# Kernel optimization log

Hardware: AMD Instinct MI355X
Metric: run time of the kernel (lower is better)

Reference implementation:

```python
import jax, jax.numpy as jnp
import numpy as np
import math

DENOM = 32.0

# e3nn scalar_activation normalizes the activation to unit second moment under N(0,1).
# Compute the gelu normalization constant by Gauss-Hermite quadrature.
_zs, _ws = np.polynomial.hermite_e.hermegauss(64)
_g = 0.5 * _zs * (1.0 + np.array([math.erf(z / math.sqrt(2.0)) for z in _zs]))
C_GELU = float(1.0 / math.sqrt((_ws * _g * _g).sum() / math.sqrt(2.0 * math.pi)))


def _spherical_harmonics(r):
    # r: [E,3] unit vectors. Component-normalized real SH for l=1,2,3.
    x, y, z = r[..., 0], r[..., 1], r[..., 2]
    s3, s5, s15 = math.sqrt(3.0), math.sqrt(5.0), math.sqrt(15.0)
    s7, s105 = math.sqrt(7.0), math.sqrt(105.0)
    s35_8, s21_8 = math.sqrt(35.0 / 8.0), math.sqrt(21.0 / 8.0)
    Y1 = s3 * r                                                     # [E,3]
    Y2 = jnp.stack([s15 * x * y, s15 * y * z, 0.5 * s5 * (3 * z * z - 1),
                    s15 * x * z, 0.5 * s15 * (x * x - y * y)], -1)   # [E,5]
    Y3 = jnp.stack([s35_8 * y * (3 * x * x - y * y), s105 * x * y * z,
                    s21_8 * y * (5 * z * z - 1), 0.5 * s7 * z * (5 * z * z - 3),
                    s21_8 * x * (5 * z * z - 1), 0.5 * s105 * z * (x * x - y * y),
                    s35_8 * x * (x * x - 3 * y * y)], -1)            # [E,7]
    return [Y1, Y2, Y3]


def setup_inputs() -> dict:
    key = jax.random.key(0)
    k = jax.random.split(key, 7)
    N, E, MUL, TMUL = 32768, 1048576, 16, 32
    return {
        "x": jax.random.normal(k[0], (N, MUL), jnp.float32),
        "positions": jax.random.normal(k[1], (N, 3), jnp.float32),
        "W_pre": jax.random.normal(k[2], (4, MUL, TMUL), jnp.float32),
        "W_post": jax.random.normal(k[3], (4, TMUL, TMUL), jnp.float32),
        "W_shortcut": jax.random.normal(k[4], (MUL, TMUL), jnp.float32),
        "senders": jax.random.randint(k[5], (E,), 0, N, jnp.int32),
        "receivers": jax.random.randint(k[6], (E,), 0, N, jnp.int32),
    }


def reference(x, positions, W_pre, W_post, W_shortcut, senders, receivers):
    N, mul = x.shape
    tmul = W_pre.shape[-1]
    # --- edge update: sh of relative positions, tensor product with sender scalars ---
    rvec = positions[receivers] - positions[senders]                 # [E,3]
    n = jnp.linalg.norm(rvec, axis=-1, keepdims=True)
    rhat = rvec / jnp.where(n == 0, 1.0, n)
    Ys = _spherical_harmonics(rhat)
    s = x[senders]                                                   # [E,mul] (0e)
    # --- aggregate edge features at receivers (segment sum) ---
    agg = [jax.ops.segment_sum(s, receivers, num_segments=N)]        # 0e block
    for Y in Ys:
        e = (s[:, :, None] * Y[:, None, :]).reshape(s.shape[0], -1)  # 0e x l -> l
        agg.append(jax.ops.segment_sum(e, receivers, num_segments=N).reshape(N, mul, Y.shape[-1]))
    # --- node update: linear_pre -> scalar act -> linear_post, plus shortcut ---
    inv_in = 1.0 / math.sqrt(mul)
    inv_mid = 1.0 / math.sqrt(tmul)
    out = []
    for l in range(4):
        a = agg[l] / DENOM
        if l == 0:
            p = (a @ W_pre[0]) * inv_in
            p = C_GELU * jax.nn.gelu(p, approximate=False)           # act on 0e scalars only
            q = (p @ W_post[0]) * inv_mid
            q = q + (x @ W_shortcut) * inv_in                        # shortcut: only 0e path exists
            out.append(q)
        else:
            p = jnp.einsum('nui,uv->nvi', a, W_pre[l]) * inv_in
            q = jnp.einsum('nvi,vw->nwi', p, W_post[l]) * inv_mid
            out.append(q.reshape(N, -1))
    return jnp.concatenate(out, axis=-1)                              # [N, tmul*16]
```

## Files before the change

kernel.cpp:

```cpp
#include <hip/hip_runtime.h>
#include <math.h>

#define NN 32768
#define EN 1048576
#define NBIN 256
#define BINCAP 8192
#define TILE 4096

#define C_GELU_F 1.5335262f

__global__ __launch_bounds__(256) void bin_k(const int* __restrict__ snd,
                                             const int* __restrict__ rcv,
                                             int* __restrict__ bin_cur,
                                             unsigned* __restrict__ binbuf) {
    __shared__ unsigned cnt[NBIN];
    __shared__ unsigned excl[NBIN];
    __shared__ unsigned cur2[NBIN];
    __shared__ unsigned gbase[NBIN];
    __shared__ unsigned stage[TILE];
    int t = threadIdx.x;
    int tile = blockIdx.x * TILE;
    cnt[t] = 0; cur2[t] = 0;
    __syncthreads();

    unsigned w[TILE / 256];
#pragma unroll
    for (int i = 0; i < TILE / 256; ++i) {
        int e = tile + i * 256 + t;
        unsigned r = (unsigned)rcv[e], s = (unsigned)snd[e];
        w[i] = (r << 15) | s;
        atomicAdd(&cnt[w[i] >> 22], 1u);
    }
    __syncthreads();

    unsigned my = cnt[t];
    excl[t] = my;
    __syncthreads();
    for (int d = 1; d < NBIN; d <<= 1) {
        unsigned v = (t >= d) ? excl[t - d] : 0u;
        __syncthreads();
        excl[t] += v;
        __syncthreads();
    }
    unsigned myexcl = excl[t] - my;
    gbase[t] = atomicAdd((unsigned*)&bin_cur[t], my);
    __syncthreads();
    excl[t] = myexcl;
    __syncthreads();

#pragma unroll
    for (int i = 0; i < TILE / 256; ++i) {
        unsigned b = w[i] >> 22;
        unsigned p = excl[b] + atomicAdd(&cur2[b], 1u);
        stage[p] = w[i];
    }
    __syncthreads();

    for (int p = t; p < TILE; p += 256) {
        unsigned ww = stage[p];
        unsigned b = ww >> 22;
        unsigned idx = gbase[b] + ((unsigned)p - excl[b]);
        if (idx < BINCAP) binbuf[b * BINCAP + idx] = ww;
    }
}

__global__ __launch_bounds__(256) void scan_k(const int* __restrict__ bin_cur,
                                              int* __restrict__ bin_start) {
    __shared__ unsigned sc[NBIN];
    int t = threadIdx.x;
    unsigned my = (unsigned)bin_cur[t];
    sc[t] = my;
    __syncthreads();
    for (int d = 1; d < NBIN; d <<= 1) {
        unsigned v = (t >= d) ? sc[t - d] : 0u;
        __syncthreads();
        sc[t] += v;
        __syncthreads();
    }
    bin_start[t] = (int)(sc[t] - my);
}

__global__ __launch_bounds__(256) void csr_k(const int* __restrict__ bin_cur,
                                             const int* __restrict__ bin_start,
                                             const unsigned* __restrict__ binbuf,
                                             int* __restrict__ row_ptr,
                                             int* __restrict__ edge_csr) {
    __shared__ unsigned cnt[128];
    __shared__ unsigned excl[128];
    __shared__ unsigned cur2[128];
    int b = blockIdx.x;
    int t = threadIdx.x;
    int M = bin_cur[b]; M = M > BINCAP ? BINCAP : M;
    int base = bin_start[b];
    if (t < 128) { cnt[t] = 0; cur2[t] = 0; }
    __syncthreads();

    const unsigned* bb = binbuf + b * BINCAP;
    for (int i = t; i < M; i += 256)
        atomicAdd(&cnt[(bb[i] >> 15) & 127], 1u);
    __syncthreads();

    if (t < 128) excl[t] = cnt[t];
    __syncthreads();
    for (int d = 1; d < 128; d <<= 1) {
        unsigned v = (t >= d && t < 128) ? excl[t - d] : 0u;
        __syncthreads();
        if (t < 128) excl[t] += v;
        __syncthreads();
    }
    if (t < 128) {
        unsigned e = excl[t] - cnt[t];
        excl[t] = e;
        row_ptr[(b << 7) + t] = base + (int)e;
        if (b == NBIN - 1 && t == 127) row_ptr[NN] = base + (int)(e + cnt[127]);
    }
    __syncthreads();

    for (int i = t; i < M; i += 256) {
        unsigned ww = bb[i];
        unsigned r7 = (ww >> 15) & 127;
        unsigned dst = excl[r7] + atomicAdd(&cur2[r7], 1u);
        edge_csr[base + dst] = (int)(ww & 0x7FFF);
    }
}

__global__ __launch_bounds__(256) void pos_k(const float* __restrict__ pos,
                                             float4* __restrict__ posw) {
    int n = blockIdx.x * 256 + threadIdx.x;
    posw[n] = make_float4(pos[3*n], pos[3*n+1], pos[3*n+2], 0.f);
}

#define TSTRIDE 17
#define NSTRIDE (16 * TSTRIDE)

__global__ __launch_bounds__(256) void fused_k(const float* __restrict__ x,
                                               const float4* __restrict__ posw,
                                               const int* __restrict__ row_ptr,
                                               const int* __restrict__ edge_csr,
                                               const float* __restrict__ Wpre,
                                               const float* __restrict__ Wpost,
                                               const float* __restrict__ Wsc,
                                               float* __restrict__ out) {
    __shared__ float sPre[4*516];
    __shared__ float sPost[4*1028];
    __shared__ float sSc[512];
    __shared__ float sT[16 * NSTRIDE];

    int t = threadIdx.x;
    for (int idx = t; idx < 2048; idx += 256)
        sPre[(idx >> 9)*516 + (idx & 511)] = Wpre[idx];
    for (int idx = t; idx < 4096; idx += 256)
        sPost[(idx >> 10)*1028 + (idx & 1023)] = Wpost[idx];
    sSc[t] = Wsc[t];
    sSc[t + 256] = Wsc[t + 256];

    int nl = t >> 4;
    int n  = blockIdx.x * 16 + nl;
    int u  = t & 15;
    int beg = row_ptr[n], end = row_ptr[n + 1];
    int cnt = end - beg;
    float4 rp = posw[n];
    float acc[16];
#pragma unroll
    for (int j = 0; j < 16; ++j) acc[j] = 0.f;

    const float s3   = 1.7320508075688772f;
    const float s5   = 2.2360679774997896f;
    const float s15  = 3.8729833462074170f;
    const float s7   = 2.6457513110645907f;
    const float s105 = 10.246950765959598f;
    const float s35_8 = 2.0916500663351889f;
    const float s21_8 = 1.6201851746019651f;

    int cl = cnt > 0 ? cnt - 1 : 0;
    int sA = edge_csr[beg];
    int sB = edge_csr[beg + (1 < cl ? 1 : cl)];
    float4 spA = posw[sA];
    float  xvA = x[(sA << 4) + u];

    for (int k = 0; k < cnt; ++k) {
        int    s  = sA;
        float4 sp = spA;
        float  sv = xvA;
        sA = sB;
        int k2 = k + 2; k2 = k2 < cl ? k2 : cl;
        sB = edge_csr[beg + k2];
        spA = posw[sA];
        xvA = x[(sA << 4) + u];

        float vx = rp.x - sp.x, vy = rp.y - sp.y, vz = rp.z - sp.z;
        float n2 = vx*vx + vy*vy + vz*vz;
        float inv;
        if (n2 > 0.f) {
            inv = rsqrtf(n2);
            inv = inv * (1.5f - 0.5f * n2 * inv * inv);
        } else inv = 0.f;
        float X = vx*inv, Y = vy*inv, Z = vz*inv;
        float XX = X*X, YY = Y*Y, ZZ = Z*Z;

        acc[0]  += sv;
        acc[1]  += sv * (s3*X);
        acc[2]  += sv * (s3*Y);
        acc[3]  += sv * (s3*Z);
        acc[4]  += sv * (s15*X*Y);
        acc[5]  += sv * (s15*Y*Z);
        acc[6]  += sv * (0.5f*s5*(3.f*ZZ - 1.f));
        acc[7]  += sv * (s15*X*Z);
        acc[8]  += sv * (0.5f*s15*(XX - YY));
        acc[9]  += sv * (s35_8*Y*(3.f*XX - YY));
        acc[10] += sv * (s105*X*Y*Z);
        acc[11] += sv * (s21_8*Y*(5.f*ZZ - 1.f));
        acc[12] += sv * (0.5f*s7*Z*(5.f*ZZ - 3.f));
        acc[13] += sv * (s21_8*X*(5.f*ZZ - 1.f));
        acc[14] += sv * (0.5f*s105*Z*(XX - YY));
        acc[15] += sv * (s35_8*X*(XX - 3.f*YY));
    }

    float* tp = sT + nl * NSTRIDE + u * TSTRIDE;
#pragma unroll
    for (int j = 0; j < 16; ++j) tp[j] = acc[j];
    __syncthreads();

    int j = t & 15;
    int l, i, offl, deg;
    if (j == 0)      { l = 0; i = 0;     offl = 0;   deg = 1; }
    else if (j < 4)  { l = 1; i = j - 1; offl = 32;  deg = 3; }
    else if (j < 9)  { l = 2; i = j - 4; offl = 128; deg = 5; }
    else             { l = 3; i = j - 9; offl = 288; deg = 7; }

    const float c1 = 0.0078125f;
    const float c2 = 0.17677669529663687f;

    const float* ap = sT + nl * NSTRIDE + j;
    float p[32];
#pragma unroll
    for (int v = 0; v < 32; ++v) p[v] = 0.f;
    const float* wp = sPre + l * 516;
#pragma unroll
    for (int uu = 0; uu < 16; ++uu) {
        float a = ap[uu * TSTRIDE];
        const float4* w4 = (const float4*)(wp + (uu << 5));
#pragma unroll
        for (int vq = 0; vq < 8; ++vq) {
            float4 w = w4[vq];
            p[4*vq+0] += a * w.x;
            p[4*vq+1] += a * w.y;
            p[4*vq+2] += a * w.z;
            p[4*vq+3] += a * w.w;
        }
    }
#pragma unroll
    for (int v = 0; v < 32; ++v) p[v] *= c1;

    if (j == 0) {
#pragma unroll
        for (int v = 0; v < 32; ++v) {
            float pv = p[v];
            p[v] = C_GELU_F * 0.5f * pv * (1.f + erff(pv * 0.7071067811865476f));
        }
    }

    float q[32];
#pragma unroll
    for (int w = 0; w < 32; ++w) q[w] = 0.f;
    const float* wq = sPost + l * 1028;
#pragma unroll
    for (int v = 0; v < 32; ++v) {
        float pv = p[v];
        const float4* w4 = (const float4*)(wq + (v << 5));
#pragma unroll
        for (int wd = 0; wd < 8; ++wd) {
            float4 w = w4[wd];
            q[4*wd+0] += pv * w.x;
            q[4*wd+1] += pv * w.y;
            q[4*wd+2] += pv * w.z;
            q[4*wd+3] += pv * w.w;
        }
    }
#pragma unroll
    for (int w = 0; w < 32; ++w) q[w] *= c2;

    if (j == 0) {
        const float* xp = x + (n << 4);
#pragma unroll
        for (int uu = 0; uu < 16; ++uu) {
            float xv = 0.25f * xp[uu];
            const float4* w4 = (const float4*)(sSc + (uu << 5));
#pragma unroll
            for (int wd = 0; wd < 8; ++wd) {
                float4 w = w4[wd];
                q[4*wd+0] += xv * w.x;
                q[4*wd+1] += xv * w.y;
                q[4*wd+2] += xv * w.z;
                q[4*wd+3] += xv * w.w;
            }
        }
    }

    float* op = out + (n << 9) + offl + i;
#pragma unroll
    for (int w = 0; w < 32; ++w) op[w * deg] = q[w];
}

extern "C" void kernel_launch(void* const* d_in, const int* in_sizes, int n_in,
                              void* d_out, int out_size, void* d_ws, size_t ws_size,
                              hipStream_t stream) {
    const float* x     = (const float*)d_in[0];
    const float* pos   = (const float*)d_in[1];
    const float* Wpre  = (const float*)d_in[2];
    const float* Wpost = (const float*)d_in[3];
    const float* Wsc   = (const float*)d_in[4];
    const int*   snd   = (const int*)d_in[5];
    const int*   rcv   = (const int*)d_in[6];
    float* out = (float*)d_out;

    char* ws = (char*)d_ws;
    int*      bin_cur   = (int*)(ws);
    int*      bin_start = (int*)(ws + 1024);
    int*      row_ptr   = (int*)(ws + 2048);
    float4*   posw      = (float4*)(ws + 0x30000);
    int*      edge_csr  = (int*)(ws + 0xB0000);
    unsigned* binbuf    = (unsigned*)(ws + 0x500000);

    hipMemsetAsync(bin_cur, 0, NBIN * sizeof(int), stream);
    bin_k<<<EN / TILE, 256, 0, stream>>>(snd, rcv, bin_cur, binbuf);
    scan_k<<<1, 256, 0, stream>>>(bin_cur, bin_start);
    csr_k<<<NBIN, 256, 0, stream>>>(bin_cur, bin_start, binbuf, row_ptr, edge_csr);
    pos_k<<<NN / 256, 256, 0, stream>>>(pos, posw);
    fused_k<<<NN / 16, 256, 0, stream>>>(x, posw, row_ptr, edge_csr,
                                         Wpre, Wpost, Wsc, out);
}
```

Baseline: 232.5 us.

## Parallelize edge SH across lanes and accumulate per-output-channel in fused kernel

The fused kernel now has each 16-lane group compute spherical harmonics for 16 edges in parallel, one edge per lane, and stage them in shared memory. Each lane then accumulates one SH component across all 16 input channels, with the sender id broadcast by shuffle and x read as float4 rows. This removes the redundant per-lane SH recomputation and the accumulator transpose through shared memory. Block sizes grow for the fused, binning and CSR kernels, at the cost of more registers and partial-chunk lane waste for low-degree nodes.

```diff
diff --git a/kernel.cpp b/kernel.cpp
--- a/kernel.cpp
+++ b/kernel.cpp
@@ -9,7 +9,7 @@
 
 #define C_GELU_F 1.5335262f
 
-__global__ __launch_bounds__(256) void bin_k(const int* __restrict__ snd,
+__global__ __launch_bounds__(512) void bin_k(const int* __restrict__ snd,
                                              const int* __restrict__ rcv,
                                              int* __restrict__ bin_cur,
                                              unsigned* __restrict__ binbuf) {
@@ -20,43 +20,44 @@
     __shared__ unsigned stage[TILE];
     int t = threadIdx.x;
     int tile = blockIdx.x * TILE;
-    cnt[t] = 0; cur2[t] = 0;
-    __syncthreads();
-
-    unsigned w[TILE / 256];
-#pragma unroll
-    for (int i = 0; i < TILE / 256; ++i) {
-        int e = tile + i * 256 + t;
+    if (t < NBIN) { cnt[t] = 0; cur2[t] = 0; }
+    __syncthreads();
+
+    unsigned w[TILE / 512];
+#pragma unroll
+    for (int i = 0; i < TILE / 512; ++i) {
+        int e = tile + i * 512 + t;
         unsigned r = (unsigned)rcv[e], s = (unsigned)snd[e];
         w[i] = (r << 15) | s;
         atomicAdd(&cnt[w[i] >> 22], 1u);
     }
     __syncthreads();
 
-    unsigned my = cnt[t];
-    excl[t] = my;
+    unsigned my = (t < NBIN) ? cnt[t] : 0u;
+    if (t < NBIN) excl[t] = my;
     __syncthreads();
     for (int d = 1; d < NBIN; d <<= 1) {
-        unsigned v = (t >= d) ? excl[t - d] : 0u;
-        __syncthreads();
-        excl[t] += v;
-        __syncthreads();
-    }
-    unsigned myexcl = excl[t] - my;
-    gbase[t] = atomicAdd((unsigned*)&bin_cur[t], my);
-    __syncthreads();
-    excl[t] = myexcl;
-    __syncthreads();
-
-#pragma unroll
-    for (int i = 0; i < TILE / 256; ++i) {
+        unsigned v = (t < NBIN && t >= d) ? excl[t - d] : 0u;
+        __syncthreads();
+        if (t < NBIN) excl[t] += v;
+        __syncthreads();
+    }
+    if (t < NBIN) {
+        unsigned myexcl = excl[t] - my;
+        gbase[t] = atomicAdd((unsigned*)&bin_cur[t], my);
+        excl[t] = myexcl;
+    }
+    __syncthreads();
+
+#pragma unroll
+    for (int i = 0; i < TILE / 512; ++i) {
         unsigned b = w[i] >> 22;
         unsigned p = excl[b] + atomicAdd(&cur2[b], 1u);
         stage[p] = w[i];
     }
     __syncthreads();
 
-    for (int p = t; p < TILE; p += 256) {
+    for (int p = t; p < TILE; p += 512) {
         unsigned ww = stage[p];
         unsigned b = ww >> 22;
         unsigned idx = gbase[b] + ((unsigned)p - excl[b]);
@@ -80,11 +81,11 @@
     bin_start[t] = (int)(sc[t] - my);
 }
 
-__global__ __launch_bounds__(256) void csr_k(const int* __restrict__ bin_cur,
-                                             const int* __restrict__ bin_start,
-                                             const unsigned* __restrict__ binbuf,
-                                             int* __restrict__ row_ptr,
-                                             int* __restrict__ edge_csr) {
+__global__ __launch_bounds__(1024) void csr_k(const int* __restrict__ bin_cur,
+                                              const int* __restrict__ bin_start,
+                                              const unsigned* __restrict__ binbuf,
+                                              int* __restrict__ row_ptr,
+                                              int* __restrict__ edge_csr) {
     __shared__ unsigned cnt[128];
     __shared__ unsigned excl[128];
     __shared__ unsigned cur2[128];
@@ -96,7 +97,7 @@
     __syncthreads();
 
     const unsigned* bb = binbuf + b * BINCAP;
-    for (int i = t; i < M; i += 256)
+    for (int i = t; i < M; i += 1024)
         atomicAdd(&cnt[(bb[i] >> 15) & 127], 1u);
     __syncthreads();
 
@@ -116,7 +117,7 @@
     }
     __syncthreads();
 
-    for (int i = t; i < M; i += 256) {
+    for (int i = t; i < M; i += 1024) {
         unsigned ww = bb[i];
         unsigned r7 = (ww >> 15) & 127;
         unsigned dst = excl[r7] + atomicAdd(&cur2[r7], 1u);
@@ -130,39 +131,38 @@
     posw[n] = make_float4(pos[3*n], pos[3*n+1], pos[3*n+2], 0.f);
 }
 
-#define TSTRIDE 17
-#define NSTRIDE (16 * TSTRIDE)
-
-__global__ __launch_bounds__(256) void fused_k(const float* __restrict__ x,
-                                               const float4* __restrict__ posw,
-                                               const int* __restrict__ row_ptr,
-                                               const int* __restrict__ edge_csr,
-                                               const float* __restrict__ Wpre,
-                                               const float* __restrict__ Wpost,
-                                               const float* __restrict__ Wsc,
-                                               float* __restrict__ out) {
+#define GROUPS 32
+#define BLK 512
+#define YST 20
+#define GST (16*YST + 8)
+
+__global__ __launch_bounds__(512, 4) void fused_k(const float* __restrict__ x,
+                                                  const float4* __restrict__ posw,
+                                                  const int* __restrict__ row_ptr,
+                                                  const int* __restrict__ edge_csr,
+                                                  const float* __restrict__ Wpre,
+                                                  const float* __restrict__ Wpost,
+                                                  const float* __restrict__ Wsc,
+                                                  float* __restrict__ out) {
     __shared__ float sPre[4*516];
     __shared__ float sPost[4*1028];
     __shared__ float sSc[512];
-    __shared__ float sT[16 * NSTRIDE];
+    __shared__ float sY[GROUPS * GST];
 
     int t = threadIdx.x;
-    for (int idx = t; idx < 2048; idx += 256)
+    for (int idx = t; idx < 2048; idx += BLK)
         sPre[(idx >> 9)*516 + (idx & 511)] = Wpre[idx];
-    for (int idx = t; idx < 4096; idx += 256)
+    for (int idx = t; idx < 4096; idx += BLK)
         sPost[(idx >> 10)*1028 + (idx & 1023)] = Wpost[idx];
     sSc[t] = Wsc[t];
-    sSc[t + 256] = Wsc[t + 256];
-
-    int nl = t >> 4;
-    int n  = blockIdx.x * 16 + nl;
-    int u  = t & 15;
+
+    int g = t >> 4;
+    int j = t & 15;
+    int n = blockIdx.x * GROUPS + g;
     int beg = row_ptr[n], end = row_ptr[n + 1];
     int cnt = end - beg;
     float4 rp = posw[n];
-    float acc[16];
-#pragma unroll
-    for (int j = 0; j < 16; ++j) acc[j] = 0.f;
+    float* yg = sY + g * GST;
 
     const float s3   = 1.7320508075688772f;
     const float s5   = 2.2360679774997896f;
@@ -172,22 +172,18 @@
     const float s35_8 = 2.0916500663351889f;
     const float s21_8 = 1.6201851746019651f;
 
-    int cl = cnt > 0 ? cnt - 1 : 0;
-    int sA = edge_csr[beg];
-    int sB = edge_csr[beg + (1 < cl ? 1 : cl)];
-    float4 spA = posw[sA];
-    float  xvA = x[(sA << 4) + u];
-
-    for (int k = 0; k < cnt; ++k) {
-        int    s  = sA;
-        float4 sp = spA;
-        float  sv = xvA;
-        sA = sB;
-        int k2 = k + 2; k2 = k2 < cl ? k2 : cl;
-        sB = edge_csr[beg + k2];
-        spA = posw[sA];
-        xvA = x[(sA << 4) + u];
-
+    float acc[16];
+#pragma unroll
+    for (int u = 0; u < 16; ++u) acc[u] = 0.f;
+
+    int nch = (cnt + 15) >> 4;
+    for (int c = 0; c < nch; ++c) {
+        int rem = cnt - (c << 4); rem = rem > 16 ? 16 : rem;
+
+        int k = (c << 4) + j;
+        int ki = k < cnt ? k : cnt - 1;
+        int sE = edge_csr[beg + ki];
+        float4 sp = posw[sE];
         float vx = rp.x - sp.x, vy = rp.y - sp.y, vz = rp.z - sp.z;
         float n2 = vx*vx + vy*vy + vz*vz;
         float inv;
@@ -198,30 +194,37 @@
         float X = vx*inv, Y = vy*inv, Z = vz*inv;
         float XX = X*X, YY = Y*Y, ZZ = Z*Z;
 
-        acc[0]  += sv;
-        acc[1]  += sv * (s3*X);
-        acc[2]  += sv * (s3*Y);
-        acc[3]  += sv * (s3*Z);
-        acc[4]  += sv * (s15*X*Y);
-        acc[5]  += sv * (s15*Y*Z);
-        acc[6]  += sv * (0.5f*s5*(3.f*ZZ - 1.f));
-        acc[7]  += sv * (s15*X*Z);
-        acc[8]  += sv * (0.5f*s15*(XX - YY));
-        acc[9]  += sv * (s35_8*Y*(3.f*XX - YY));
-        acc[10] += sv * (s105*X*Y*Z);
-        acc[11] += sv * (s21_8*Y*(5.f*ZZ - 1.f));
-        acc[12] += sv * (0.5f*s7*Z*(5.f*ZZ - 3.f));
-        acc[13] += sv * (s21_8*X*(5.f*ZZ - 1.f));
-        acc[14] += sv * (0.5f*s105*Z*(XX - YY));
-        acc[15] += sv * (s35_8*X*(XX - 3.f*YY));
-    }
-
-    float* tp = sT + nl * NSTRIDE + u * TSTRIDE;
-#pragma unroll
-    for (int j = 0; j < 16; ++j) tp[j] = acc[j];
-    __syncthreads();
-
-    int j = t & 15;
+        float* yr = yg + j * YST;
+        ((float4*)yr)[0] = make_float4(1.f, s3*X, s3*Y, s3*Z);
+        ((float4*)yr)[1] = make_float4(s15*X*Y, s15*Y*Z,
+                                       0.5f*s5*(3.f*ZZ - 1.f), s15*X*Z);
+        ((float4*)yr)[2] = make_float4(0.5f*s15*(XX - YY),
+                                       s35_8*Y*(3.f*XX - YY),
+                                       s105*X*Y*Z,
+                                       s21_8*Y*(5.f*ZZ - 1.f));
+        ((float4*)yr)[3] = make_float4(0.5f*s7*Z*(5.f*ZZ - 3.f),
+                                       s21_8*X*(5.f*ZZ - 1.f),
+                                       0.5f*s105*Z*(XX - YY),
+                                       s35_8*X*(XX - 3.f*YY));
+
+#pragma unroll 4
+        for (int e = 0; e < rem; ++e) {
+            int se = __shfl(sE, (t & 48) + e, 64);
+            float y = yg[e * YST + j];
+            const float4* xp = (const float4*)(x + (se << 4));
+            float4 a0 = xp[0], a1 = xp[1], a2 = xp[2], a3 = xp[3];
+            acc[0]  += a0.x * y;  acc[1]  += a0.y * y;
+            acc[2]  += a0.z * y;  acc[3]  += a0.w * y;
+            acc[4]  += a1.x * y;  acc[5]  += a1.y * y;
+            acc[6]  += a1.z * y;  acc[7]  += a1.w * y;
+            acc[8]  += a2.x * y;  acc[9]  += a2.y * y;
+            acc[10] += a2.z * y;  acc[11] += a2.w * y;
+            acc[12] += a3.x * y;  acc[13] += a3.y * y;
+            acc[14] += a3.z * y;  acc[15] += a3.w * y;
+        }
+    }
+    __syncthreads();
+
     int l, i, offl, deg;
     if (j == 0)      { l = 0; i = 0;     offl = 0;   deg = 1; }
     else if (j < 4)  { l = 1; i = j - 1; offl = 32;  deg = 3; }
@@ -231,14 +234,13 @@
     const float c1 = 0.0078125f;
     const float c2 = 0.17677669529663687f;
 
-    const float* ap = sT + nl * NSTRIDE + j;
     float p[32];
 #pragma unroll
     for (int v = 0; v < 32; ++v) p[v] = 0.f;
     const float* wp = sPre + l * 516;
 #pragma unroll
     for (int uu = 0; uu < 16; ++uu) {
-        float a = ap[uu * TSTRIDE];
+        float a = acc[uu];
         const float4* w4 = (const float4*)(wp + (uu << 5));
 #pragma unroll
         for (int vq = 0; vq < 8; ++vq) {
@@ -323,10 +325,10 @@
     unsigned* binbuf    = (unsigned*)(ws + 0x500000);
 
     hipMemsetAsync(bin_cur, 0, NBIN * sizeof(int), stream);
-    bin_k<<<EN / TILE, 256, 0, stream>>>(snd, rcv, bin_cur, binbuf);
+    bin_k<<<EN / TILE, 512, 0, stream>>>(snd, rcv, bin_cur, binbuf);
     scan_k<<<1, 256, 0, stream>>>(bin_cur, bin_start);
-    csr_k<<<NBIN, 256, 0, stream>>>(bin_cur, bin_start, binbuf, row_ptr, edge_csr);
+    csr_k<<<NBIN, 1024, 0, stream>>>(bin_cur, bin_start, binbuf, row_ptr, edge_csr);
     pos_k<<<NN / 256, 256, 0, stream>>>(pos, posw);
-    fused_k<<<NN / 16, 256, 0, stream>>>(x, posw, row_ptr, edge_csr,
-                                         Wpre, Wpost, Wsc, out);
-}
+    fused_k<<<NN / GROUPS, BLK, 0, stream>>>(x, posw, row_ptr, edge_csr,
+                                             Wpre, Wpost, Wsc, out);
+}
```

Measured after the change: 197.9 us. -14.9%, faster.
